# Performance work log

Hardware: AMD Instinct MI355X
Metric: run time of the kernel (lower is better)

Reference implementation:

```python
import jax, jax.numpy as jnp
import numpy as np
import math

B, T, C, NH, NL, AD, V, BS, MT = 32, 50, 128, 8, 6, 64, 18, 150, 4096
HD = C // NH


def setup_inputs():
    key = jax.random.key(0)
    ks = jax.random.split(key, 32)
    w = lambda i, shape, s=0.02: (jax.random.normal(ks[i], shape) * s).astype(jnp.float32)
    d = {}
    d["states"] = jax.random.uniform(ks[0], (B, T, 4, 84, 84), jnp.float32)
    d["rtgs"] = jax.random.normal(ks[1], (B, T, 1), jnp.float32)
    d["actions"] = jax.random.randint(ks[2], (B, T, 1), 0, V)
    d["timesteps"] = jax.random.randint(ks[3], (B, 1, 1), 0, MT)
    d["targets"] = jax.random.randint(ks[4], (B, T, 1), 0, V)
    d["pos_emb"] = w(5, (1, BS + 1, C))
    d["global_pos_emb"] = w(6, (1, MT + 1, C))
    d["c1_w"] = w(7, (32, 4, 8, 8)); d["c1_b"] = w(8, (32,), 0.01)
    d["c2_w"] = w(9, (64, 32, 4, 4)); d["c2_b"] = w(10, (64,), 0.01)
    d["c3_w"] = w(11, (64, 64, 3, 3)); d["c3_b"] = w(12, (64,), 0.01)
    d["enc_w"] = w(13, (C, 3136)); d["enc_b"] = w(14, (C,), 0.01)
    d["ret_w"] = w(15, (C, 1)); d["ret_b"] = w(16, (C,), 0.01)
    d["act_tab"] = w(17, (V, C))
    d["ln_w"] = jnp.ones((NL, 3, C), jnp.float32)
    d["ln_b"] = jnp.zeros((NL, 3, C), jnp.float32)
    d["attn_w"] = w(18, (NL, 4, C, C)); d["attn_b"] = w(19, (NL, 4, C), 0.01)
    d["mlp_w1"] = w(20, (NL, 4 * C, C)); d["mlp_b1"] = w(21, (NL, 4 * C), 0.01)
    d["mlp_w2"] = w(22, (NL, C, 4 * C)); d["mlp_b2"] = w(23, (NL, C), 0.01)
    d["ad_dw"] = w(24, (NL, AD, C), 1e-3); d["ad_db"] = jnp.zeros((NL, AD), jnp.float32)
    d["ad_uw"] = w(25, (NL, C, AD), 1e-3); d["ad_ub"] = jnp.zeros((NL, C), jnp.float32)
    d["lnf_w"] = jnp.ones((C,), jnp.float32); d["lnf_b"] = jnp.zeros((C,), jnp.float32)
    d["head_w"] = w(26, (V, C))
    return d


def _ln(x, g, b):
    m = jnp.mean(x, -1, keepdims=True)
    v = jnp.mean(jnp.square(x - m), -1, keepdims=True)
    return (x - m) * jax.lax.rsqrt(v + 1e-5) * g + b


def _conv(x, w, b, s):
    y = jax.lax.conv_general_dilated(x, w, (s, s), "VALID", dimension_numbers=("NCHW", "OIHW", "NCHW"))
    return y + b[None, :, None, None]


def _forward(states, rtgs, pos_emb, global_pos_emb, c1_w, c1_b, c2_w, c2_b, c3_w, c3_b,
             enc_w, enc_b, ret_w, ret_b, act_tab, ln_w, ln_b, attn_w, attn_b,
             mlp_w1, mlp_b1, mlp_w2, mlp_b2, ad_dw, ad_db, ad_uw, ad_ub,
             lnf_w, lnf_b, head_w, actions, timesteps):
    # state encoder (conv stem): [B*T,4,84,84] -> [B,T,C]
    x = states.reshape(-1, 4, 84, 84)
    x = jax.nn.relu(_conv(x, c1_w, c1_b, 4))  # -> 20x20
    x = jax.nn.relu(_conv(x, c2_w, c2_b, 2))  # -> 9x9
    x = jax.nn.relu(_conv(x, c3_w, c3_b, 1))  # -> 7x7
    x = x.reshape(x.shape[0], -1)             # 64*7*7 = 3136
    state_e = jnp.tanh(x @ enc_w.T + enc_b).reshape(B, T, C)
    rtg_e = jnp.tanh(rtgs @ ret_w.T + ret_b)
    act_e = jnp.tanh(act_tab[actions[..., 0]])
    # interleave rtg/state/action at [::3],[1::3],[2::3]
    tok = jnp.stack([rtg_e, state_e, act_e], axis=2).reshape(B, 3 * T, C)
    S = 3 * T
    pe = global_pos_emb[0][timesteps[:, 0, 0]][:, None, :] + pos_emb[:, :S, :]
    h = tok + pe  # drop = identity in eval
    mask = jnp.tril(jnp.ones((S, S), bool))
    scale = 1.0 / math.sqrt(HD)
    for l in range(NL):
        normed = _ln(h, ln_w[l, 2], ln_b[l, 2])           # ln3 on pre-block input
        xa = _ln(h, ln_w[l, 0], ln_b[l, 0])               # ln1
        k = (xa @ attn_w[l, 0].T + attn_b[l, 0]).reshape(B, S, NH, HD)
        q = (xa @ attn_w[l, 1].T + attn_b[l, 1]).reshape(B, S, NH, HD)
        v = (xa @ attn_w[l, 2].T + attn_b[l, 2]).reshape(B, S, NH, HD)
        att = jnp.einsum("bihd,bjhd->bhij", q, k) * scale
        att = jax.nn.softmax(jnp.where(mask, att, -jnp.inf), axis=-1)
        y = jnp.einsum("bhij,bjhd->bihd", att, v).reshape(B, S, C)
        h1 = h + y @ attn_w[l, 3].T + attn_b[l, 3]
        xm = _ln(h1, ln_w[l, 1], ln_b[l, 1])              # ln2
        f = h1 + jax.nn.gelu(xm @ mlp_w1[l].T + mlp_b1[l], approximate=False) @ mlp_w2[l].T + mlp_b2[l]
        ad = jax.nn.relu(normed @ ad_dw[l].T + ad_db[l]) @ ad_uw[l].T + ad_ub[l]
        h = h1 + f + ad                                   # x = hidden + drop(forward) + adapter
    logits = _ln(h, lnf_w, lnf_b) @ head_w.T
    return logits[:, 1::3, :]  # predictions from state tokens


def reference(states, rtgs, pos_emb, global_pos_emb, c1_w, c1_b, c2_w, c2_b, c3_w, c3_b,
              enc_w, enc_b, ret_w, ret_b, act_tab, ln_w, ln_b, attn_w, attn_b,
              mlp_w1, mlp_b1, mlp_w2, mlp_b2, ad_dw, ad_db, ad_uw, ad_ub,
              lnf_w, lnf_b, head_w, actions, timesteps, targets):
    # targets only toggles sequence layout (not None here) and the CE loss; logits are the kernel payload
    return _forward(states, rtgs, pos_emb, global_pos_emb, c1_w, c1_b, c2_w, c2_b, c3_w, c3_b,
                    enc_w, enc_b, ret_w, ret_b, act_tab, ln_w, ln_b, attn_w, attn_b,
                    mlp_w1, mlp_b1, mlp_w2, mlp_b2, ad_dw, ad_db, ad_uw, ad_ub,
                    lnf_w, lnf_b, head_w, actions, timesteps)
```

## Files before the change

### kernel.cpp

```cpp
#include <hip/hip_runtime.h>
#include <hip/hip_bf16.h>
#include <math.h>

typedef __hip_bfloat16 bf16;

typedef __attribute__((ext_vector_type(8))) short bfrag;
typedef __attribute__((ext_vector_type(4))) float f32x4;
union FragU { bfrag s; uint2 d[2]; unsigned int u[4]; };

static __device__ __forceinline__ float b2f(bf16 x){ return __bfloat162float(x); }
static __device__ __forceinline__ unsigned int f2b2(float lo, float hi){
  bf16 l = __float2bfloat16(lo), h = __float2bfloat16(hi);
  unsigned short lb, hb;
  __builtin_memcpy(&lb, &l, 2); __builtin_memcpy(&hb, &h, 2);
  return (unsigned int)lb | ((unsigned int)hb << 16);
}
static __device__ __forceinline__ void sto(float* p, size_t i, float v){ p[i] = v; }
static __device__ __forceinline__ void sto(bf16* p, size_t i, float v){ p[i] = __float2bfloat16(v); }

constexpr size_t MiB = 1ull << 20;
constexpr size_t OFF_C1   = 0;
constexpr size_t OFF_C2   = 41*MiB;
constexpr size_t OFF_C3   = 58*MiB;
constexpr size_t OFF_SE   = 69*MiB;
constexpr size_t OFF_H    = 0;
constexpr size_t OFF_XA   = 3*MiB;
constexpr size_t OFF_NORM = 6*MiB;
constexpr size_t OFF_QKV  = 9*MiB;
constexpr size_t OFF_Y    = 17*MiB;
constexpr size_t OFF_H1   = 20*MiB;
constexpr size_t OFF_MLPH = 23*MiB;
constexpr size_t OFF_ADH  = 33*MiB;
constexpr size_t OFF_WT   = 0;
constexpr size_t OFF_WT1  = OFF_C2;

__global__ __launch_bounds__(256) void c1wt_kernel(const float* __restrict__ w, bf16* __restrict__ wt)
{
  int i = blockIdx.x*256 + threadIdx.x;
  wt[i] = __float2bfloat16(w[i]);
}

__global__ __launch_bounds__(256) void conv1_kernel(
    const float* __restrict__ x, const bf16* __restrict__ wt,
    const float* __restrict__ bias, bf16* __restrict__ out)
{
  __shared__ bf16 ost[32*408];
  int b = blockIdx.x;
  int t = threadIdx.x;
  int lane = t & 63, wave = t >> 6;
  int quad = lane >> 4, r16 = lane & 15;
  const float* xb = x + (size_t)b*28224;
  const float* pb[7];
  #pragma unroll
  for (int i = 0; i < 7; ++i){
    int tile = wave*7 + i; if (tile > 24) tile = 24;
    int m = tile*16 + r16;
    int oy = m / 20, ox = m % 20;
    pb[i] = xb + 4*oy*84 + 4*ox;
  }
  f32x4 acc[7][2];
  #pragma unroll
  for (int i = 0; i < 7; ++i)
    #pragma unroll
    for (int j = 0; j < 2; ++j) acc[i][j] = (f32x4){0.f,0.f,0.f,0.f};
  for (int kc = 0; kc < 8; ++kc){
    int c = kc >> 1, ky = (kc & 1)*4 + quad;
    int off = c*7056 + ky*84;
    FragU bf_[2];
    #pragma unroll
    for (int tn = 0; tn < 2; ++tn){
      uint4 wv = *(const uint4*)(wt + (tn*16 + r16)*256 + kc*32 + quad*8);
      bf_[tn].u[0] = wv.x; bf_[tn].u[1] = wv.y; bf_[tn].u[2] = wv.z; bf_[tn].u[3] = wv.w;
    }
    #pragma unroll
    for (int i = 0; i < 7; ++i){
      if (wave*7 + i < 25){
        const float* p = pb[i] + off;
        float4 fa = *(const float4*)p;
        float4 fb = *(const float4*)(p + 4);
        FragU a;
        a.u[0] = f2b2(fa.x, fa.y); a.u[1] = f2b2(fa.z, fa.w);
        a.u[2] = f2b2(fb.x, fb.y); a.u[3] = f2b2(fb.z, fb.w);
        acc[i][0] = __builtin_amdgcn_mfma_f32_16x16x32_bf16(a.s, bf_[0].s, acc[i][0], 0, 0, 0);
        acc[i][1] = __builtin_amdgcn_mfma_f32_16x16x32_bf16(a.s, bf_[1].s, acc[i][1], 0, 0, 0);
      }
    }
  }
  #pragma unroll
  for (int i = 0; i < 7; ++i){
    int tile = wave*7 + i;
    if (tile < 25){
      int m0 = tile*16 + quad*4;
      #pragma unroll
      for (int tn = 0; tn < 2; ++tn){
        int oc = tn*16 + r16;
        float bb = bias[oc];
        float v0 = fmaxf(acc[i][tn][0] + bb, 0.f);
        float v1 = fmaxf(acc[i][tn][1] + bb, 0.f);
        float v2 = fmaxf(acc[i][tn][2] + bb, 0.f);
        float v3 = fmaxf(acc[i][tn][3] + bb, 0.f);
        *(uint2*)(ost + oc*408 + m0) = make_uint2(f2b2(v0, v1), f2b2(v2, v3));
      }
    }
  }
  __syncthreads();
  bf16* outp = out + (size_t)b*12800;
  for (int e = t; e < 1600; e += 256){
    int oc = e / 50, col = e % 50;
    uint4 v = *(const uint4*)(ost + oc*408 + col*8);
    *(uint4*)(outp + oc*400 + col*8) = v;
  }
}

__global__ __launch_bounds__(256) void conv2_kernel(
    const bf16* __restrict__ x, const float* __restrict__ w,
    const float* __restrict__ bias, bf16* __restrict__ out)
{
  __shared__ bf16 xs2[32*20*24];
  int b = blockIdx.x;
  int t = threadIdx.x;
  const unsigned int* xb = (const unsigned int*)(x + (size_t)b*12800);
  for (int p = t; p < 6400; p += 256){
    int c = p / 200, rem = p % 200;
    int r = rem / 10, cp = rem % 10;
    ((unsigned int*)xs2)[((c*20 + r)*24 + 2*cp) >> 1] = xb[p];
  }
  __syncthreads();
  int lane = t & 63, wave = t >> 6;
  int quad = lane >> 4, r16 = lane & 15;
  int oc = wave*16 + r16;
  f32x4 acc[6];
  #pragma unroll
  for (int i = 0; i < 6; ++i) acc[i] = (f32x4){0.f,0.f,0.f,0.f};
  for (int kc = 0; kc < 16; ++kc){
    const float* wp = w + oc*512 + kc*32 + quad*8;
    float4 wa = ((const float4*)wp)[0], wb = ((const float4*)wp)[1];
    FragU bfr;
    bfr.u[0] = f2b2(wa.x, wa.y); bfr.u[1] = f2b2(wa.z, wa.w);
    bfr.u[2] = f2b2(wb.x, wb.y); bfr.u[3] = f2b2(wb.z, wb.w);
    int c = kc*2 + (quad >> 1);
    int ky0 = (quad & 1)*2;
    #pragma unroll
    for (int tile = 0; tile < 6; ++tile){
      int m = tile*16 + r16; if (m > 80) m = 80;
      int oy = m / 9, ox = m % 9;
      int idx1 = (c*20 + 2*oy + ky0)*24 + 2*ox;
      const unsigned int* q1 = (const unsigned int*)(xs2 + idx1);
      const unsigned int* q2 = (const unsigned int*)(xs2 + idx1 + 24);
      FragU a;
      a.u[0] = q1[0]; a.u[1] = q1[1];
      a.u[2] = q2[0]; a.u[3] = q2[1];
      acc[tile] = __builtin_amdgcn_mfma_f32_16x16x32_bf16(a.s, bfr.s, acc[tile], 0, 0, 0);
    }
  }
  __syncthreads();
  float bb = bias[oc];
  #pragma unroll
  for (int tile = 0; tile < 6; ++tile){
    #pragma unroll
    for (int r = 0; r < 4; ++r){
      int m = tile*16 + quad*4 + r;
      if (m < 81){
        float v = fmaxf(acc[tile][r] + bb, 0.f);
        xs2[oc*81 + m] = __float2bfloat16(v);
      }
    }
  }
  __syncthreads();
  const unsigned int* lsu = (const unsigned int*)xs2;
  unsigned int* op = (unsigned int*)(out + (size_t)b*5184);
  for (int e = t; e < 2592; e += 256) op[e] = lsu[e];
}

__global__ __launch_bounds__(256) void wt_kernel(const float* __restrict__ w, bf16* __restrict__ wt)
{
  int o = blockIdx.x*256 + threadIdx.x;
  int oc = o / 576, r = o % 576;
  int tap = r >> 6, c = r & 63;
  wt[o] = __float2bfloat16(w[oc*576 + c*9 + tap]);
}

__global__ __launch_bounds__(256) void conv3_kernel(
    const bf16* __restrict__ x, const bf16* __restrict__ wt,
    const float* __restrict__ bias, bf16* __restrict__ out)
{
  __shared__ ushort lin[5184];
  __shared__ ushort xt[81*72];
  int b = blockIdx.x;
  int t = threadIdx.x;
  const uint2* xb = (const uint2*)(x + (size_t)b*5184);
  for (int i = t; i < 1296; i += 256) ((uint2*)lin)[i] = xb[i];
  __syncthreads();
  for (int e = t; e < 5184; e += 256){
    int c = e & 63, p = e >> 6;
    xt[p*72 + c] = lin[c*81 + p];
  }
  __syncthreads();
  int lane = t & 63, wv = t >> 6;
  int quad = lane >> 4, r16 = lane & 15;
  int m = wv*16 + r16;
  int pos = m < 49 ? m : 48;
  int pb = (pos/7)*9 + (pos%7);
  const ushort* abase = xt + pb*72 + quad*8;
  const bf16* wb0 = wt + (size_t)r16*576 + quad*8;
  f32x4 acc[4];
  #pragma unroll
  for (int tn = 0; tn < 4; ++tn) acc[tn] = (f32x4){0.f,0.f,0.f,0.f};
  #pragma unroll 3
  for (int kc = 0; kc < 18; ++kc){
    int tap = kc >> 1;
    int toff = (tap/3)*9 + (tap%3);
    int soff = toff*72 + (kc & 1)*32;
    FragU a;
    uint4 av = *(const uint4*)(abase + soff);
    a.u[0] = av.x; a.u[1] = av.y; a.u[2] = av.z; a.u[3] = av.w;
    #pragma unroll
    for (int tn = 0; tn < 4; ++tn){
      uint4 bv = *(const uint4*)(wb0 + tn*9216 + kc*32);
      FragU bfr;
      bfr.u[0] = bv.x; bfr.u[1] = bv.y; bfr.u[2] = bv.z; bfr.u[3] = bv.w;
      acc[tn] = __builtin_amdgcn_mfma_f32_16x16x32_bf16(a.s, bfr.s, acc[tn], 0, 0, 0);
    }
  }
  __syncthreads();
  #pragma unroll
  for (int tn = 0; tn < 4; ++tn){
    int oc = tn*16 + r16;
    float bb = bias[oc];
    #pragma unroll
    for (int r = 0; r < 4; ++r){
      int p = wv*16 + quad*4 + r;
      if (p < 49){
        bf16 v = __float2bfloat16(fmaxf(acc[tn][r] + bb, 0.f));
        ushort u; __builtin_memcpy(&u, &v, 2);
        lin[oc*49 + p] = u;
      }
    }
  }
  __syncthreads();
  uint2* op = (uint2*)(out + (size_t)b*3136);
  for (int e = t; e < 784; e += 256) op[e] = ((const uint2*)lin)[e];
}

template<int ACT, typename OT>
__global__ __launch_bounds__(256) void mgemm(
    const bf16* __restrict__ X, const float* __restrict__ W,
    const float* __restrict__ bias, const float* __restrict__ add, float add_scale,
    OT* __restrict__ out, int M, int N, int K)
{
  __shared__ bf16 Xs[64*40];
  __shared__ bf16 Ws[64*40];
  int nb = N >> 6;
  int bn = (blockIdx.x % nb) << 6;
  int bm = (blockIdx.x / nb) << 6;
  int t = threadIdx.x;
  int lane = t & 63, wave = t >> 6;
  int mw = wave >> 1, nw = wave & 1;
  int quad = lane >> 4, r16 = lane & 15;
  int srow = t >> 2, scol = (t & 3)*8;
  f32x4 acc[2][2];
  #pragma unroll
  for (int i = 0; i < 2; ++i)
    #pragma unroll
    for (int j = 0; j < 2; ++j) acc[i][j] = (f32x4){0.f,0.f,0.f,0.f};
  for (int k0 = 0; k0 < K; k0 += 32){
    uint4 xv = *(const uint4*)(X + (size_t)(bm + srow)*K + k0 + scol);
    uint2* xd = (uint2*)(Xs + srow*40 + scol);
    xd[0] = make_uint2(xv.x, xv.y); xd[1] = make_uint2(xv.z, xv.w);
    const float* wp = W + (size_t)(bn + srow)*K + k0 + scol;
    float4 wa = ((const float4*)wp)[0], wb = ((const float4*)wp)[1];
    uint2* wd = (uint2*)(Ws + srow*40 + scol);
    wd[0] = make_uint2(f2b2(wa.x, wa.y), f2b2(wa.z, wa.w));
    wd[1] = make_uint2(f2b2(wb.x, wb.y), f2b2(wb.z, wb.w));
    __syncthreads();
    FragU af[2], bf_[2];
    #pragma unroll
    for (int tm = 0; tm < 2; ++tm){
      const bf16* p = Xs + (mw*32 + tm*16 + r16)*40 + quad*8;
      af[tm].d[0] = *(const uint2*)p; af[tm].d[1] = *(const uint2*)(p + 4);
    }
    #pragma unroll
    for (int tn = 0; tn < 2; ++tn){
      const bf16* p = Ws + (nw*32 + tn*16 + r16)*40 + quad*8;
      bf_[tn].d[0] = *(const uint2*)p; bf_[tn].d[1] = *(const uint2*)(p + 4);
    }
    #pragma unroll
    for (int tm = 0; tm < 2; ++tm)
      #pragma unroll
      for (int tn = 0; tn < 2; ++tn)
        acc[tm][tn] = __builtin_amdgcn_mfma_f32_16x16x32_bf16(af[tm].s, bf_[tn].s, acc[tm][tn], 0, 0, 0);
    __syncthreads();
  }
  #pragma unroll
  for (int tm = 0; tm < 2; ++tm){
    #pragma unroll
    for (int tn = 0; tn < 2; ++tn){
      int n = bn + nw*32 + tn*16 + r16;
      float bb = bias[n];
      #pragma unroll
      for (int r = 0; r < 4; ++r){
        int m = bm + mw*32 + tm*16 + quad*4 + r;
        float v = acc[tm][tn][r] + bb;
        if (ACT == 1) v = tanhf(v);
        else if (ACT == 2) v = 0.5f*v*(1.0f + erff(v*0.70710678118f));
        else if (ACT == 3) v = fmaxf(v, 0.f);
        if (add) v += add_scale * add[(size_t)m*N + n];
        sto(out, (size_t)m*N + n, v);
      }
    }
  }
}

__global__ __launch_bounds__(256) void token_kernel(
    const float* __restrict__ rtgs, const int* __restrict__ actions, const int* __restrict__ timesteps,
    const float* __restrict__ ret_w, const float* __restrict__ ret_b, const float* __restrict__ act_tab,
    const float* __restrict__ pos_emb, const float* __restrict__ gpe,
    const float* __restrict__ se, float* __restrict__ h)
{
  int idx = blockIdx.x*256 + threadIdx.x;
  int c = idx & 127; int row = idx >> 7;
  int s = row % 150; int b = row / 150;
  int t = s / 3; int r = s - 3*t;
  float tok;
  if (r == 0)      tok = tanhf(rtgs[b*50+t] * ret_w[c] + ret_b[c]);
  else if (r == 1) tok = se[(b*50+t)*128 + c];
  else             tok = tanhf(act_tab[actions[b*50+t]*128 + c]);
  float pe = gpe[(size_t)timesteps[b]*128 + c] + pos_emb[s*128 + c];
  h[idx] = tok + pe;
}

__global__ __launch_bounds__(256) void ln_kernel(
    const float* __restrict__ x,
    const float* __restrict__ g1, const float* __restrict__ be1, bf16* __restrict__ o1,
    const float* __restrict__ g2, const float* __restrict__ be2, bf16* o2)
{
  int lane = threadIdx.x & 63;
  int row = blockIdx.x*4 + (threadIdx.x >> 6);
  const float2 xv = *(const float2*)(x + (size_t)row*128 + lane*2);
  float s = xv.x + xv.y, sq = xv.x*xv.x + xv.y*xv.y;
  #pragma unroll
  for (int off = 32; off; off >>= 1){ s += __shfl_xor(s, off); sq += __shfl_xor(sq, off); }
  float mean = s * 0.0078125f;
  float var  = sq * 0.0078125f - mean*mean;
  float rstd = rsqrtf(var + 1e-5f);
  float n0 = (xv.x - mean)*rstd, n1 = (xv.y - mean)*rstd;
  int c0 = lane*2;
  ((unsigned int*)o1)[row*64 + lane] = f2b2(n0*g1[c0] + be1[c0], n1*g1[c0+1] + be1[c0+1]);
  if (o2)
    ((unsigned int*)o2)[row*64 + lane] = f2b2(n0*g2[c0] + be2[c0], n1*g2[c0+1] + be2[c0+1]);
}

__global__ __launch_bounds__(256) void attn_kernel(const bf16* __restrict__ qkv, bf16* __restrict__ y)
{
  int bh = blockIdx.x;
  int hh = bh & 7; int b = bh >> 3;
  __shared__ float ks[150*16];
  __shared__ float vs[150*16];
  int t = threadIdx.x;
  for (int i = t; i < 2400; i += 256){
    int s = i >> 4; int d = i & 15;
    const bf16* base = qkv + (size_t)(b*150 + s)*384;
    ks[i] = b2f(base[hh*16 + d]);
    vs[i] = b2f(base[256 + hh*16 + d]);
  }
  __syncthreads();
  if (t < 150){
    const bf16* qr = qkv + (size_t)(b*150 + t)*384 + 128 + hh*16;
    float q[16];
    #pragma unroll
    for (int d = 0; d < 16; ++d) q[d] = b2f(qr[d]) * 0.25f;
    float m = -1e30f, l = 0.f, acc[16] = {};
    for (int j = 0; j <= t; ++j){
      const float* kr = ks + j*16;
      float s = 0.f;
      #pragma unroll
      for (int d = 0; d < 16; ++d) s += q[d]*kr[d];
      float mn = fmaxf(m, s);
      float corr = __expf(m - mn);
      float p = __expf(s - mn);
      l = l*corr + p;
      const float* vr = vs + j*16;
      #pragma unroll
      for (int d = 0; d < 16; ++d) acc[d] = acc[d]*corr + p*vr[d];
      m = mn;
    }
    float inv = 1.f / l;
    bf16* yr = y + (size_t)(b*150 + t)*128 + hh*16;
    #pragma unroll
    for (int d = 0; d < 16; ++d) yr[d] = __float2bfloat16(acc[d]*inv);
  }
}

__global__ __launch_bounds__(64) void head_kernel(
    const float* __restrict__ h, const float* __restrict__ g, const float* __restrict__ be,
    const float* __restrict__ hw, float* __restrict__ out)
{
  int bt = blockIdx.x;
  int lane = threadIdx.x;
  int b = bt / 50, t = bt % 50;
  const float* row = h + ((size_t)b*150 + 3*t + 1)*128;
  float2 xv = *(const float2*)(row + lane*2);
  float s = xv.x + xv.y, sq = xv.x*xv.x + xv.y*xv.y;
  #pragma unroll
  for (int off = 32; off; off >>= 1){ s += __shfl_xor(s, off); sq += __shfl_xor(sq, off); }
  float mean = s * 0.0078125f;
  float var  = sq * 0.0078125f - mean*mean;
  float rstd = rsqrtf(var + 1e-5f);
  int c0 = lane*2;
  __shared__ float sh[128];
  sh[c0]   = (xv.x-mean)*rstd*g[c0]   + be[c0];
  sh[c0+1] = (xv.y-mean)*rstd*g[c0+1] + be[c0+1];
  __syncthreads();
  if (lane < 18){
    const float* wr = hw + lane*128;
    float acc = 0.f;
    #pragma unroll
    for (int c = 0; c < 128; c += 4){
      float4 wf = *(const float4*)(wr + c);
      acc += sh[c]*wf.x + sh[c+1]*wf.y + sh[c+2]*wf.z + sh[c+3]*wf.w;
    }
    out[bt*18 + lane] = acc;
  }
}

extern "C" void kernel_launch(void* const* d_in, const int* in_sizes, int n_in,
                              void* d_out, int out_size, void* d_ws, size_t ws_size,
                              hipStream_t stream)
{
  const float* states    = (const float*)d_in[0];
  const float* rtgs      = (const float*)d_in[1];
  const int*   actions   = (const int*)d_in[2];
  const int*   timesteps = (const int*)d_in[3];
  const float* pos_emb   = (const float*)d_in[5];
  const float* gpe       = (const float*)d_in[6];
  const float* c1_w = (const float*)d_in[7];  const float* c1_b = (const float*)d_in[8];
  const float* c2_w = (const float*)d_in[9];  const float* c2_b = (const float*)d_in[10];
  const float* c3_w = (const float*)d_in[11]; const float* c3_b = (const float*)d_in[12];
  const float* enc_w = (const float*)d_in[13]; const float* enc_b = (const float*)d_in[14];
  const float* ret_w = (const float*)d_in[15]; const float* ret_b = (const float*)d_in[16];
  const float* act_tab = (const float*)d_in[17];
  const float* ln_w = (const float*)d_in[18]; const float* ln_b = (const float*)d_in[19];
  const float* attn_w = (const float*)d_in[20]; const float* attn_b = (const float*)d_in[21];
  const float* mlp_w1 = (const float*)d_in[22]; const float* mlp_b1 = (const float*)d_in[23];
  const float* mlp_w2 = (const float*)d_in[24]; const float* mlp_b2 = (const float*)d_in[25];
  const float* ad_dw = (const float*)d_in[26]; const float* ad_db = (const float*)d_in[27];
  const float* ad_uw = (const float*)d_in[28]; const float* ad_ub = (const float*)d_in[29];
  const float* lnf_w = (const float*)d_in[30]; const float* lnf_b = (const float*)d_in[31];
  const float* head_w = (const float*)d_in[32];
  float* out = (float*)d_out;

  char* ws = (char*)d_ws;
  bf16* c1o  = (bf16*)(ws + OFF_C1);
  bf16* c2o  = (bf16*)(ws + OFF_C2);
  bf16* c3o  = (bf16*)(ws + OFF_C3);
  float* se  = (float*)(ws + OFF_SE);
  float* h   = (float*)(ws + OFF_H);
  bf16* xa   = (bf16*)(ws + OFF_XA);
  bf16* nrm  = (bf16*)(ws + OFF_NORM);
  bf16* qkv  = (bf16*)(ws + OFF_QKV);
  bf16* y    = (bf16*)(ws + OFF_Y);
  float* h1  = (float*)(ws + OFF_H1);
  bf16* mlph = (bf16*)(ws + OFF_MLPH);
  bf16* adh  = (bf16*)(ws + OFF_ADH);
  bf16* wtb  = (bf16*)(ws + OFF_WT);
  bf16* wt1  = (bf16*)(ws + OFF_WT1);

  c1wt_kernel<<<32, 256, 0, stream>>>(c1_w, wt1);
  conv1_kernel<<<1600, 256, 0, stream>>>(states, wt1, c1_b, c1o);
  conv2_kernel<<<1600, 256, 0, stream>>>(c1o, c2_w, c2_b, c2o);
  wt_kernel<<<144, 256, 0, stream>>>(c3_w, wtb);
  conv3_kernel<<<1600, 256, 0, stream>>>(c2o, wtb, c3_b, c3o);
  mgemm<1, float><<<25*2, 256, 0, stream>>>(c3o, enc_w, enc_b, nullptr, 0.f, se, 1600, 128, 3136);
  token_kernel<<<2400, 256, 0, stream>>>(rtgs, actions, timesteps, ret_w, ret_b, act_tab,
                                         pos_emb, gpe, se, h);

  for (int l = 0; l < 6; ++l){
    const float* g1 = ln_w + (l*3+0)*128; const float* be1 = ln_b + (l*3+0)*128;
    const float* g2 = ln_w + (l*3+1)*128; const float* be2 = ln_b + (l*3+1)*128;
    const float* g3 = ln_w + (l*3+2)*128; const float* be3 = ln_b + (l*3+2)*128;
    ln_kernel<<<1200, 256, 0, stream>>>(h, g1, be1, xa, g3, be3, nrm);
    mgemm<0, bf16><<<75*6, 256, 0, stream>>>(xa, attn_w + (size_t)l*4*16384, attn_b + l*4*128,
                                             nullptr, 0.f, qkv, 4800, 384, 128);
    attn_kernel<<<256, 256, 0, stream>>>(qkv, y);
    mgemm<0, float><<<75*2, 256, 0, stream>>>(y, attn_w + ((size_t)l*4+3)*16384, attn_b + (l*4+3)*128,
                                              h, 1.0f, h1, 4800, 128, 128);
    ln_kernel<<<1200, 256, 0, stream>>>(h1, g2, be2, xa, nullptr, nullptr, nullptr);
    mgemm<2, bf16><<<75*8, 256, 0, stream>>>(xa, mlp_w1 + (size_t)l*65536, mlp_b1 + l*512,
                                             nullptr, 0.f, mlph, 4800, 512, 128);
    mgemm<3, bf16><<<75*1, 256, 0, stream>>>(nrm, ad_dw + (size_t)l*8192, ad_db + l*64,
                                             nullptr, 0.f, adh, 4800, 64, 128);
    mgemm<0, float><<<75*2, 256, 0, stream>>>(mlph, mlp_w2 + (size_t)l*65536, mlp_b2 + l*128,
                                              h1, 2.0f, h, 4800, 128, 512);
    mgemm<0, float><<<75*2, 256, 0, stream>>>(adh, ad_uw + (size_t)l*8192, ad_ub + l*128,
                                              h, 1.0f, h, 4800, 128, 64);
  }
  head_kernel<<<1600, 64, 0, stream>>>(h, lnf_w, lnf_b, head_w, out);
}
```

Before: 1.087 ms.

## Split conv1 into quarter-image blocks with async global-to-LDS input staging

Conv1 now launches four blocks per image, each covering five output rows. Each block stages its 4x24x84 float input slab into shared memory with global_load_lds before computing, instead of every lane reading overlapping 8x8 patches directly from global memory. This is meant to raise parallelism and occupancy and to cut redundant global traffic. The cost is that overlapping input rows are loaded by adjacent blocks, and a 16-row tile that straddles the block boundary is partly wasted and clamped.

```diff
diff --git a/kernel.cpp b/kernel.cpp
--- a/kernel.cpp
+++ b/kernel.cpp
@@ -17,6 +17,13 @@
 }
 static __device__ __forceinline__ void sto(float* p, size_t i, float v){ p[i] = v; }
 static __device__ __forceinline__ void sto(bf16* p, size_t i, float v){ p[i] = __float2bfloat16(v); }
+
+static __device__ __forceinline__ void gld_lds16(const void* g, void* l){
+  __builtin_amdgcn_global_load_lds(
+      (const __attribute__((address_space(1))) unsigned int*)g,
+      (__attribute__((address_space(3))) unsigned int*)l,
+      16, 0, 0);
+}
 
 constexpr size_t MiB = 1ull << 20;
 constexpr size_t OFF_C1   = 0;
@@ -44,28 +51,25 @@
     const float* __restrict__ x, const bf16* __restrict__ wt,
     const float* __restrict__ bias, bf16* __restrict__ out)
 {
-  __shared__ bf16 ost[32*408];
-  int b = blockIdx.x;
+  __shared__ float xsf[4*24*84];
+  int bi = blockIdx.x;
+  int b = bi >> 2, hf = bi & 3;
   int t = threadIdx.x;
+  const char* xb = (const char*)(x + (size_t)b*28224 + hf*20*84);
+  for (int i = t; i < 2016; i += 256){
+    int c = i / 504, rem = i % 504;
+    gld_lds16(xb + (size_t)c*28224 + (size_t)rem*16, ((char*)xsf) + (size_t)i*16);
+  }
+  __syncthreads();
   int lane = t & 63, wave = t >> 6;
   int quad = lane >> 4, r16 = lane & 15;
-  const float* xb = x + (size_t)b*28224;
-  const float* pb[7];
-  #pragma unroll
-  for (int i = 0; i < 7; ++i){
-    int tile = wave*7 + i; if (tile > 24) tile = 24;
-    int m = tile*16 + r16;
-    int oy = m / 20, ox = m % 20;
-    pb[i] = xb + 4*oy*84 + 4*ox;
-  }
-  f32x4 acc[7][2];
-  #pragma unroll
-  for (int i = 0; i < 7; ++i)
+  f32x4 acc[2][2];
+  #pragma unroll
+  for (int i = 0; i < 2; ++i)
     #pragma unroll
     for (int j = 0; j < 2; ++j) acc[i][j] = (f32x4){0.f,0.f,0.f,0.f};
   for (int kc = 0; kc < 8; ++kc){
     int c = kc >> 1, ky = (kc & 1)*4 + quad;
-    int off = c*7056 + ky*84;
     FragU bf_[2];
     #pragma unroll
     for (int tn = 0; tn < 2; ++tn){
@@ -73,9 +77,12 @@
       bf_[tn].u[0] = wv.x; bf_[tn].u[1] = wv.y; bf_[tn].u[2] = wv.z; bf_[tn].u[3] = wv.w;
     }
     #pragma unroll
-    for (int i = 0; i < 7; ++i){
-      if (wave*7 + i < 25){
-        const float* p = pb[i] + off;
+    for (int i = 0; i < 2; ++i){
+      int tile = i*4 + wave;
+      if (tile < 7){
+        int m = tile*16 + r16; if (m > 99) m = 99;
+        int oy = m / 20, ox = m % 20;
+        const float* p = xsf + (c*24 + 4*oy + ky)*84 + 4*ox;
         float4 fa = *(const float4*)p;
         float4 fb = *(const float4*)(p + 4);
         FragU a;
@@ -86,29 +93,32 @@
       }
     }
   }
-  #pragma unroll
-  for (int i = 0; i < 7; ++i){
-    int tile = wave*7 + i;
-    if (tile < 25){
+  __syncthreads();
+  bf16* ost = (bf16*)xsf;
+  #pragma unroll
+  for (int i = 0; i < 2; ++i){
+    int tile = i*4 + wave;
+    if (tile < 7){
       int m0 = tile*16 + quad*4;
-      #pragma unroll
-      for (int tn = 0; tn < 2; ++tn){
-        int oc = tn*16 + r16;
-        float bb = bias[oc];
-        float v0 = fmaxf(acc[i][tn][0] + bb, 0.f);
-        float v1 = fmaxf(acc[i][tn][1] + bb, 0.f);
-        float v2 = fmaxf(acc[i][tn][2] + bb, 0.f);
-        float v3 = fmaxf(acc[i][tn][3] + bb, 0.f);
-        *(uint2*)(ost + oc*408 + m0) = make_uint2(f2b2(v0, v1), f2b2(v2, v3));
+      if (m0 < 100){
+        #pragma unroll
+        for (int tn = 0; tn < 2; ++tn){
+          int oc = tn*16 + r16;
+          float bb = bias[oc];
+          float v0 = fmaxf(acc[i][tn][0] + bb, 0.f);
+          float v1 = fmaxf(acc[i][tn][1] + bb, 0.f);
+          float v2 = fmaxf(acc[i][tn][2] + bb, 0.f);
+          float v3 = fmaxf(acc[i][tn][3] + bb, 0.f);
+          *(uint2*)(ost + oc*104 + m0) = make_uint2(f2b2(v0, v1), f2b2(v2, v3));
+        }
       }
     }
   }
   __syncthreads();
-  bf16* outp = out + (size_t)b*12800;
-  for (int e = t; e < 1600; e += 256){
-    int oc = e / 50, col = e % 50;
-    uint4 v = *(const uint4*)(ost + oc*408 + col*8);
-    *(uint4*)(outp + oc*400 + col*8) = v;
+  bf16* outp = out + (size_t)b*12800 + hf*100;
+  for (int e = t; e < 800; e += 256){
+    int oc = e / 25, g = e % 25;
+    *(uint2*)(outp + oc*400 + g*4) = *(const uint2*)(ost + oc*104 + g*4);
   }
 }
 
@@ -466,7 +476,7 @@
   bf16* wt1  = (bf16*)(ws + OFF_WT1);
 
   c1wt_kernel<<<32, 256, 0, stream>>>(c1_w, wt1);
-  conv1_kernel<<<1600, 256, 0, stream>>>(states, wt1, c1_b, c1o);
+  conv1_kernel<<<6400, 256, 0, stream>>>(states, wt1, c1_b, c1o);
   conv2_kernel<<<1600, 256, 0, stream>>>(c1o, c2_w, c2_b, c2o);
   wt_kernel<<<144, 256, 0, stream>>>(c3_w, wtb);
   conv3_kernel<<<1600, 256, 0, stream>>>(c2o, wtb, c3_b, c3o);
```

Measured after the change: 1.096 ms. About the same (+0.8%).

## Fuse LayerNorm into GEMM prologues and merge MLP-down with adapter-up GEMM

Applied to the files above, without the earlier changes.

Adds a K=128 GEMM kernel that can run LayerNorm on fp32 rows while loading its input tile into shared memory. This removes the two separate ln_kernel launches per layer and the bf16 normalized intermediates they wrote. It also adds a dual GEMM that accumulates the MLP second projection and the adapter up-projection in one K loop with combined biases and the residual add, replacing two launches and a read-modify-write of h. In exchange, LayerNorm statistics are recomputed by every N-block of each fused GEMM, and the weight workspace offset is moved.

```diff
diff --git a/kernel.cpp b/kernel.cpp
--- a/kernel.cpp
+++ b/kernel.cpp
@@ -24,14 +24,12 @@
 constexpr size_t OFF_C3   = 58*MiB;
 constexpr size_t OFF_SE   = 69*MiB;
 constexpr size_t OFF_H    = 0;
-constexpr size_t OFF_XA   = 3*MiB;
-constexpr size_t OFF_NORM = 6*MiB;
 constexpr size_t OFF_QKV  = 9*MiB;
 constexpr size_t OFF_Y    = 17*MiB;
 constexpr size_t OFF_H1   = 20*MiB;
 constexpr size_t OFF_MLPH = 23*MiB;
 constexpr size_t OFF_ADH  = 33*MiB;
-constexpr size_t OFF_WT   = 0;
+constexpr size_t OFF_WT   = 3*MiB;
 constexpr size_t OFF_WT1  = OFF_C2;
 
 __global__ __launch_bounds__(256) void c1wt_kernel(const float* __restrict__ w, bf16* __restrict__ wt)
@@ -311,6 +309,177 @@
   }
 }
 
+template<int ACT, int LNF, typename OT>
+__global__ __launch_bounds__(256) void mgemm128(
+    const void* __restrict__ Xv, const float* __restrict__ g, const float* __restrict__ be,
+    const float* __restrict__ W, const float* __restrict__ bias,
+    const float* __restrict__ add, float add_scale,
+    OT* __restrict__ out, int M, int N)
+{
+  __shared__ bf16 Xs[64*136];
+  __shared__ bf16 Ws[64*136];
+  int nb = N >> 6;
+  int bn = (blockIdx.x % nb) << 6;
+  int bm = (blockIdx.x / nb) << 6;
+  int t = threadIdx.x;
+  int row = t >> 2, cch = (t & 3) << 5;
+  if (LNF){
+    const float* xr = (const float*)Xv + (size_t)(bm + row)*128 + cch;
+    float4 xv[8];
+    #pragma unroll
+    for (int i = 0; i < 8; ++i) xv[i] = ((const float4*)xr)[i];
+    float s = 0.f, sq = 0.f;
+    #pragma unroll
+    for (int i = 0; i < 8; ++i){
+      s  += xv[i].x + xv[i].y + xv[i].z + xv[i].w;
+      sq += xv[i].x*xv[i].x + xv[i].y*xv[i].y + xv[i].z*xv[i].z + xv[i].w*xv[i].w;
+    }
+    s += __shfl_xor(s, 1); sq += __shfl_xor(sq, 1);
+    s += __shfl_xor(s, 2); sq += __shfl_xor(sq, 2);
+    float mean = s * 0.0078125f;
+    float var  = sq * 0.0078125f - mean*mean;
+    float rstd = rsqrtf(var + 1e-5f);
+    unsigned int* xd = (unsigned int*)(Xs + row*136 + cch);
+    #pragma unroll
+    for (int i = 0; i < 8; ++i){
+      int c = cch + i*4;
+      float a0 = (xv[i].x - mean)*rstd*g[c]   + be[c];
+      float a1 = (xv[i].y - mean)*rstd*g[c+1] + be[c+1];
+      float a2 = (xv[i].z - mean)*rstd*g[c+2] + be[c+2];
+      float a3 = (xv[i].w - mean)*rstd*g[c+3] + be[c+3];
+      xd[2*i] = f2b2(a0, a1); xd[2*i+1] = f2b2(a2, a3);
+    }
+  } else {
+    const uint4* xr = (const uint4*)((const bf16*)Xv + (size_t)(bm + row)*128 + cch);
+    uint4* xd = (uint4*)(Xs + row*136 + cch);
+    #pragma unroll
+    for (int i = 0; i < 4; ++i) xd[i] = xr[i];
+  }
+  {
+    const float* wr = W + (size_t)(bn + row)*128 + cch;
+    unsigned int* wd = (unsigned int*)(Ws + row*136 + cch);
+    #pragma unroll
+    for (int i = 0; i < 8; ++i){
+      float4 wv = ((const float4*)wr)[i];
+      wd[2*i] = f2b2(wv.x, wv.y); wd[2*i+1] = f2b2(wv.z, wv.w);
+    }
+  }
+  __syncthreads();
+  int lane = t & 63, wave = t >> 6;
+  int mw = wave >> 1, nw = wave & 1;
+  int quad = lane >> 4, r16 = lane & 15;
+  f32x4 acc[2][2];
+  #pragma unroll
+  for (int i = 0; i < 2; ++i)
+    #pragma unroll
+    for (int j = 0; j < 2; ++j) acc[i][j] = (f32x4){0.f,0.f,0.f,0.f};
+  #pragma unroll
+  for (int k0 = 0; k0 < 128; k0 += 32){
+    FragU af[2], bf_[2];
+    #pragma unroll
+    for (int tm = 0; tm < 2; ++tm){
+      const bf16* p = Xs + (mw*32 + tm*16 + r16)*136 + k0 + quad*8;
+      af[tm].d[0] = *(const uint2*)p; af[tm].d[1] = *(const uint2*)(p + 4);
+    }
+    #pragma unroll
+    for (int tn = 0; tn < 2; ++tn){
+      const bf16* p = Ws + (nw*32 + tn*16 + r16)*136 + k0 + quad*8;
+      bf_[tn].d[0] = *(const uint2*)p; bf_[tn].d[1] = *(const uint2*)(p + 4);
+    }
+    #pragma unroll
+    for (int tm = 0; tm < 2; ++tm)
+      #pragma unroll
+      for (int tn = 0; tn < 2; ++tn)
+        acc[tm][tn] = __builtin_amdgcn_mfma_f32_16x16x32_bf16(af[tm].s, bf_[tn].s, acc[tm][tn], 0, 0, 0);
+  }
+  #pragma unroll
+  for (int tm = 0; tm < 2; ++tm){
+    #pragma unroll
+    for (int tn = 0; tn < 2; ++tn){
+      int n = bn + nw*32 + tn*16 + r16;
+      float bb = bias[n];
+      #pragma unroll
+      for (int r = 0; r < 4; ++r){
+        int m = bm + mw*32 + tm*16 + quad*4 + r;
+        float v = acc[tm][tn][r] + bb;
+        if (ACT == 1) v = tanhf(v);
+        else if (ACT == 2) v = 0.5f*v*(1.0f + erff(v*0.70710678118f));
+        else if (ACT == 3) v = fmaxf(v, 0.f);
+        if (add) v += add_scale * add[(size_t)m*N + n];
+        sto(out, (size_t)m*N + n, v);
+      }
+    }
+  }
+}
+
+__global__ __launch_bounds__(256) void mgemm_dual(
+    const bf16* __restrict__ X1, const float* __restrict__ W1,
+    const bf16* __restrict__ X2, const float* __restrict__ W2,
+    const float* __restrict__ b1, const float* __restrict__ b2,
+    const float* __restrict__ add, float add_scale,
+    float* __restrict__ out, int M, int N)
+{
+  __shared__ bf16 Xs[64*40];
+  __shared__ bf16 Ws[64*40];
+  int nb = N >> 6;
+  int bn = (blockIdx.x % nb) << 6;
+  int bm = (blockIdx.x / nb) << 6;
+  int t = threadIdx.x;
+  int lane = t & 63, wave = t >> 6;
+  int mw = wave >> 1, nw = wave & 1;
+  int quad = lane >> 4, r16 = lane & 15;
+  int srow = t >> 2, scol = (t & 3)*8;
+  f32x4 acc[2][2];
+  #pragma unroll
+  for (int i = 0; i < 2; ++i)
+    #pragma unroll
+    for (int j = 0; j < 2; ++j) acc[i][j] = (f32x4){0.f,0.f,0.f,0.f};
+  for (int kk = 0; kk < 18; ++kk){
+    const bf16* X; const float* W; int K; int k0;
+    if (kk < 16){ X = X1; W = W1; K = 512; k0 = kk*32; }
+    else        { X = X2; W = W2; K = 64;  k0 = (kk - 16)*32; }
+    uint4 xv = *(const uint4*)(X + (size_t)(bm + srow)*K + k0 + scol);
+    uint2* xd = (uint2*)(Xs + srow*40 + scol);
+    xd[0] = make_uint2(xv.x, xv.y); xd[1] = make_uint2(xv.z, xv.w);
+    const float* wp = W + (size_t)(bn + srow)*K + k0 + scol;
+    float4 wa = ((const float4*)wp)[0], wb = ((const float4*)wp)[1];
+    uint2* wd = (uint2*)(Ws + srow*40 + scol);
+    wd[0] = make_uint2(f2b2(wa.x, wa.y), f2b2(wa.z, wa.w));
+    wd[1] = make_uint2(f2b2(wb.x, wb.y), f2b2(wb.z, wb.w));
+    __syncthreads();
+    FragU af[2], bf_[2];
+    #pragma unroll
+    for (int tm = 0; tm < 2; ++tm){
+      const bf16* p = Xs + (mw*32 + tm*16 + r16)*40 + quad*8;
+      af[tm].d[0] = *(const uint2*)p; af[tm].d[1] = *(const uint2*)(p + 4);
+    }
+    #pragma unroll
+    for (int tn = 0; tn < 2; ++tn){
+      const bf16* p = Ws + (nw*32 + tn*16 + r16)*40 + quad*8;
+      bf_[tn].d[0] = *(const uint2*)p; bf_[tn].d[1] = *(const uint2*)(p + 4);
+    }
+    #pragma unroll
+    for (int tm = 0; tm < 2; ++tm)
+      #pragma unroll
+      for (int tn = 0; tn < 2; ++tn)
+        acc[tm][tn] = __builtin_amdgcn_mfma_f32_16x16x32_bf16(af[tm].s, bf_[tn].s, acc[tm][tn], 0, 0, 0);
+    __syncthreads();
+  }
+  #pragma unroll
+  for (int tm = 0; tm < 2; ++tm){
+    #pragma unroll
+    for (int tn = 0; tn < 2; ++tn){
+      int n = bn + nw*32 + tn*16 + r16;
+      float bb = b1[n] + b2[n];
+      #pragma unroll
+      for (int r = 0; r < 4; ++r){
+        int m = bm + mw*32 + tm*16 + quad*4 + r;
+        out[(size_t)m*N + n] = acc[tm][tn][r] + bb + add_scale * add[(size_t)m*N + n];
+      }
+    }
+  }
+}
+
 __global__ __launch_bounds__(256) void token_kernel(
     const float* __restrict__ rtgs, const int* __restrict__ actions, const int* __restrict__ timesteps,
     const float* __restrict__ ret_w, const float* __restrict__ ret_b, const float* __restrict__ act_tab,
@@ -327,27 +496,6 @@
   else             tok = tanhf(act_tab[actions[b*50+t]*128 + c]);
   float pe = gpe[(size_t)timesteps[b]*128 + c] + pos_emb[s*128 + c];
   h[idx] = tok + pe;
-}
-
-__global__ __launch_bounds__(256) void ln_kernel(
-    const float* __restrict__ x,
-    const float* __restrict__ g1, const float* __restrict__ be1, bf16* __restrict__ o1,
-    const float* __restrict__ g2, const float* __restrict__ be2, bf16* o2)
-{
-  int lane = threadIdx.x & 63;
-  int row = blockIdx.x*4 + (threadIdx.x >> 6);
-  const float2 xv = *(const float2*)(x + (size_t)row*128 + lane*2);
-  float s = xv.x + xv.y, sq = xv.x*xv.x + xv.y*xv.y;
-  #pragma unroll
-  for (int off = 32; off; off >>= 1){ s += __shfl_xor(s, off); sq += __shfl_xor(sq, off); }
-  float mean = s * 0.0078125f;
-  float var  = sq * 0.0078125f - mean*mean;
-  float rstd = rsqrtf(var + 1e-5f);
-  float n0 = (xv.x - mean)*rstd, n1 = (xv.y - mean)*rstd;
-  int c0 = lane*2;
-  ((unsigned int*)o1)[row*64 + lane] = f2b2(n0*g1[c0] + be1[c0], n1*g1[c0+1] + be1[c0+1]);
-  if (o2)
-    ((unsigned int*)o2)[row*64 + lane] = f2b2(n0*g2[c0] + be2[c0], n1*g2[c0+1] + be2[c0+1]);
 }
 
 __global__ __launch_bounds__(256) void attn_kernel(const bf16* __restrict__ qkv, bf16* __restrict__ y)
@@ -455,8 +603,6 @@
   bf16* c3o  = (bf16*)(ws + OFF_C3);
   float* se  = (float*)(ws + OFF_SE);
   float* h   = (float*)(ws + OFF_H);
-  bf16* xa   = (bf16*)(ws + OFF_XA);
-  bf16* nrm  = (bf16*)(ws + OFF_NORM);
   bf16* qkv  = (bf16*)(ws + OFF_QKV);
   bf16* y    = (bf16*)(ws + OFF_Y);
   float* h1  = (float*)(ws + OFF_H1);
@@ -478,21 +624,18 @@
     const float* g1 = ln_w + (l*3+0)*128; const float* be1 = ln_b + (l*3+0)*128;
     const float* g2 = ln_w + (l*3+1)*128; const float* be2 = ln_b + (l*3+1)*128;
     const float* g3 = ln_w + (l*3+2)*128; const float* be3 = ln_b + (l*3+2)*128;
-    ln_kernel<<<1200, 256, 0, stream>>>(h, g1, be1, xa, g3, be3, nrm);
-    mgemm<0, bf16><<<75*6, 256, 0, stream>>>(xa, attn_w + (size_t)l*4*16384, attn_b + l*4*128,
-                                             nullptr, 0.f, qkv, 4800, 384, 128);
+    mgemm128<0, 1, bf16><<<75*6, 256, 0, stream>>>(h, g1, be1,
+        attn_w + (size_t)l*4*16384, attn_b + l*4*128, nullptr, 0.f, qkv, 4800, 384);
     attn_kernel<<<256, 256, 0, stream>>>(qkv, y);
-    mgemm<0, float><<<75*2, 256, 0, stream>>>(y, attn_w + ((size_t)l*4+3)*16384, attn_b + (l*4+3)*128,
-                                              h, 1.0f, h1, 4800, 128, 128);
-    ln_kernel<<<1200, 256, 0, stream>>>(h1, g2, be2, xa, nullptr, nullptr, nullptr);
-    mgemm<2, bf16><<<75*8, 256, 0, stream>>>(xa, mlp_w1 + (size_t)l*65536, mlp_b1 + l*512,
-                                             nullptr, 0.f, mlph, 4800, 512, 128);
-    mgemm<3, bf16><<<75*1, 256, 0, stream>>>(nrm, ad_dw + (size_t)l*8192, ad_db + l*64,
-                                             nullptr, 0.f, adh, 4800, 64, 128);
-    mgemm<0, float><<<75*2, 256, 0, stream>>>(mlph, mlp_w2 + (size_t)l*65536, mlp_b2 + l*128,
-                                              h1, 2.0f, h, 4800, 128, 512);
-    mgemm<0, float><<<75*2, 256, 0, stream>>>(adh, ad_uw + (size_t)l*8192, ad_ub + l*128,
-                                              h, 1.0f, h, 4800, 128, 64);
+    mgemm128<0, 0, float><<<75*2, 256, 0, stream>>>(y, nullptr, nullptr,
+        attn_w + ((size_t)l*4+3)*16384, attn_b + (l*4+3)*128, h, 1.0f, h1, 4800, 128);
+    mgemm128<2, 1, bf16><<<75*8, 256, 0, stream>>>(h1, g2, be2,
+        mlp_w1 + (size_t)l*65536, mlp_b1 + l*512, nullptr, 0.f, mlph, 4800, 512);
+    mgemm128<3, 1, bf16><<<75*1, 256, 0, stream>>>(h, g3, be3,
+        ad_dw + (size_t)l*8192, ad_db + l*64, nullptr, 0.f, adh, 4800, 64);
+    mgemm_dual<<<75*2, 256, 0, stream>>>(mlph, mlp_w2 + (size_t)l*65536,
+        adh, ad_uw + (size_t)l*8192, mlp_b2 + l*128, ad_ub + l*128,
+        h1, 2.0f, h, 4800, 128);
   }
   head_kernel<<<1600, 64, 0, stream>>>(h, lnf_w, lnf_b, head_w, out);
 }
```

Measured after the change: 1.082 ms. No clear change (-0.5%).
